# Kernel tuning notes

Hardware: AMD Instinct MI355X
Metric: run time of the kernel (lower is better)

Reference implementation:

```python
import jax, jax.numpy as jnp
import numpy as np

EPS = 1e-6


def _rms_norm(x, w):
    # RMSNorm over last dim in fp32, like Qwen3RMSNorm
    x32 = x.astype(jnp.float32)
    var = jnp.mean(x32 * x32, axis=-1, keepdims=True)
    return (x32 * jax.lax.rsqrt(var + EPS)).astype(x.dtype) * w


def _rotate_half(x):
    h = x.shape[-1] // 2
    return jnp.concatenate([-x[..., h:], x[..., :h]], axis=-1)


def setup_inputs() -> dict:
    key = jax.random.key(0)
    ks = jax.random.split(key, 8)
    B, S, HID = 1, 8192, 1024
    H, HKV, D = 16, 8, 128
    n_seg = 8
    hidden_states = jax.random.normal(ks[0], (B, S, HID), dtype=jnp.float32)
    cu_seqlens = jnp.arange(n_seg + 1, dtype=jnp.int32) * (S // n_seg)
    # multimodal RoPE tables: two position streams, each [B, S, D]
    inv_freq = 1.0 / (1e6 ** (jnp.arange(0, D, 2, dtype=jnp.float32) / D))
    pos = jnp.arange(S, dtype=jnp.float32)
    ang0 = pos[:, None] * inv_freq[None, :]            # [S, D/2]
    ang1 = (pos[:, None] * 0.5) * inv_freq[None, :]    # second stream
    def tab(a):
        return jnp.concatenate([a, a], axis=-1)[None]   # [1, S, D]
    cos = jnp.stack([tab(jnp.cos(ang0)), tab(jnp.cos(ang1))], axis=0)  # [2,1,S,D]
    sin = jnp.stack([tab(jnp.sin(ang0)), tab(jnp.sin(ang1))], axis=0)
    sd = 0.02
    Wq = jax.random.normal(ks[1], (H * D, HID), dtype=jnp.float32) * sd
    Wk = jax.random.normal(ks[2], (HKV * D, HID), dtype=jnp.float32) * sd
    Wv = jax.random.normal(ks[3], (HKV * D, HID), dtype=jnp.float32) * sd
    Wo = jax.random.normal(ks[4], (HID, H * D), dtype=jnp.float32) * sd
    q_norm_w = 1.0 + jax.random.normal(ks[5], (D,), dtype=jnp.float32) * sd
    k_norm_w = 1.0 + jax.random.normal(ks[6], (D,), dtype=jnp.float32) * sd
    return {"hidden_states": hidden_states, "cu_seqlens": cu_seqlens,
            "cos": cos, "sin": sin, "Wq": Wq, "Wk": Wk, "Wv": Wv, "Wo": Wo,
            "q_norm_w": q_norm_w, "k_norm_w": k_norm_w}


def reference(hidden_states, cu_seqlens, cos, sin, Wq, Wk, Wv, Wo, q_norm_w, k_norm_w):
    B, S, _ = hidden_states.shape
    D = q_norm_w.shape[0]
    H = Wq.shape[0] // D
    HKV = Wk.shape[0] // D
    groups = H // HKV
    n_seg = cu_seqlens.shape[0] - 1   # equal-length segments (static)
    L = S // n_seg
    scaling = D ** -0.5

    # projections -> [B, H(kv), S, D]
    q = (hidden_states @ Wq.T).reshape(B, S, H, D).transpose(0, 2, 1, 3)
    k = (hidden_states @ Wk.T).reshape(B, S, HKV, D).transpose(0, 2, 1, 3)
    v = (hidden_states @ Wv.T).reshape(B, S, HKV, D).transpose(0, 2, 1, 3)

    q = _rms_norm(q, q_norm_w)
    k = _rms_norm(k, k_norm_w)

    # multimodal RoPE: interleave the two streams across the two half-dims
    half = D // 2
    cos_e = jnp.concatenate([cos[0, ..., :half], cos[1, ..., half:]], axis=-1)[:, None]  # [B,1,S,D]
    sin_e = jnp.concatenate([sin[0, ..., :half], sin[1, ..., half:]], axis=-1)[:, None]
    q = q * cos_e + _rotate_half(q) * sin_e
    k = k * cos_e + _rotate_half(k) * sin_e

    # GQA: repeat kv heads
    k = jnp.repeat(k, groups, axis=1)
    v = jnp.repeat(v, groups, axis=1)

    # block-diagonal attention over cu_seqlens segments (equal-length -> reshape)
    qb = q.reshape(B, H, n_seg, L, D)
    kb = k.reshape(B, H, n_seg, L, D)
    vb = v.reshape(B, H, n_seg, L, D)
    scores = jnp.einsum('bhnld,bhnmd->bhnlm', qb, kb) * scaling
    probs = jax.nn.softmax(scores, axis=-1)
    ob = jnp.einsum('bhnlm,bhnmd->bhnld', probs, vb)
    out = ob.reshape(B, H, S, D).transpose(0, 2, 1, 3).reshape(B, S, H * D)
    return out @ Wo.T
```

## Files before the change

### kernel.cpp

```cpp
#include <hip/hip_runtime.h>

#define S_LEN 8192
#define HID   1024
#define NH    16
#define NKV   8
#define HD    128
#define LSEG  1024

typedef float  f4  __attribute__((ext_vector_type(4)));
typedef _Float16 h4 __attribute__((ext_vector_type(4)));
typedef _Float16 h8 __attribute__((ext_vector_type(8)));

__device__ __forceinline__ void gl_lds16(const void* g, void* l) {
  __builtin_amdgcn_global_load_lds((const __attribute__((address_space(1))) void*)g,
                                   (__attribute__((address_space(3))) void*)l, 16, 0, 0);
}

__device__ __forceinline__ h8 ld8u(const _Float16* p) {
  h4 a = *(const h4*)p;
  h4 b = *(const h4*)(p + 4);
  return __builtin_shufflevector(a, b, 0, 1, 2, 3, 4, 5, 6, 7);
}

template <int CTRL>
__device__ __forceinline__ float dppf(float v) {
  return __builtin_bit_cast(float,
      __builtin_amdgcn_mov_dpp(__builtin_bit_cast(int, v), CTRL, 0xF, 0xF, true));
}
__device__ __forceinline__ float red16_max(float x) {
  x = fmaxf(x, dppf<0xB1>(x));
  x = fmaxf(x, dppf<0x4E>(x));
  x = fmaxf(x, dppf<0x141>(x));
  x = fmaxf(x, dppf<0x140>(x));
  return x;
}
__device__ __forceinline__ float red16_sum(float x) {
  x += dppf<0xB1>(x);
  x += dppf<0x4E>(x);
  x += dppf<0x141>(x);
  x += dppf<0x140>(x);
  return x;
}

__global__ void convert_kernel(const float* __restrict__ hid, const float* __restrict__ wq,
                               const float* __restrict__ wk, const float* __restrict__ wv,
                               const float* __restrict__ wo,
                               _Float16* __restrict__ hid16, _Float16* __restrict__ wqkv,
                               _Float16* __restrict__ wo16) {
  const int total4 = 3670016;
  for (int i = blockIdx.x * blockDim.x + threadIdx.x; i < total4; i += gridDim.x * blockDim.x) {
    int i4 = i * 4;
    const float* src; _Float16* dst;
    if      (i4 <  8388608) { src = hid + i4;              dst = hid16 + i4; }
    else if (i4 < 10485760) { src = wq + (i4 -  8388608);  dst = wqkv + (i4 - 8388608); }
    else if (i4 < 11534336) { src = wk + (i4 - 10485760);  dst = wqkv + 2097152 + (i4 - 10485760); }
    else if (i4 < 12582912) { src = wv + (i4 - 11534336);  dst = wqkv + 3145728 + (i4 - 11534336); }
    else                    { src = wo + (i4 - 12582912);  dst = wo16 + (i4 - 12582912); }
    f4 x = *(const f4*)src;
    h4 y; y[0]=(_Float16)x[0]; y[1]=(_Float16)x[1]; y[2]=(_Float16)x[2]; y[3]=(_Float16)x[3];
    *(h4*)dst = y;
  }
}

template <int FUSED>
__global__ __launch_bounds__(256, 3)
void gemm_kernel(const _Float16* __restrict__ A, const _Float16* __restrict__ B,
                 float* __restrict__ Cout, int K, int N,
                 const float* __restrict__ cosp, const float* __restrict__ sinp,
                 const float* __restrict__ qnw, const float* __restrict__ knw,
                 _Float16* __restrict__ q16, _Float16* __restrict__ k16,
                 _Float16* __restrict__ v16T) {
  __shared__ __align__(16) char smem[32768];

  constexpr int GX  = FUSED ? 32 : 8;
  constexpr int NWG = FUSED ? 2048 : 512;
  const int lin = blockIdx.y * GX + blockIdx.x;
  const int swz = (lin & 7) * (NWG >> 3) + (lin >> 3);
  const int bx = swz & (GX - 1), by = swz / GX;

  const int tid = threadIdx.x, w = tid >> 6, ln = tid & 63;
  const int l15 = ln & 15, l4 = ln >> 4;
  const int m0 = by * 128, n0 = bx * 128;
  const int sg_row = ln >> 2, sg_cho = (ln & 3) * 8;

  f4 acc[2][8] = {};

  for (int k0 = 0; k0 < K; k0 += 64) {
    __syncthreads();
#pragma unroll
    for (int r = 0; r < 2; r++) {
      int ch = r * 4 + w;
#pragma unroll
      for (int u = 0; u < 2; u++) {
        gl_lds16(A + (size_t)(m0 + ch * 16 + sg_row) * K + k0 + u * 32 + sg_cho,
                 smem + u * 8192 + ch * 1024);
        gl_lds16(B + (size_t)(n0 + ch * 16 + sg_row) * K + k0 + u * 32 + sg_cho,
                 smem + 16384 + u * 8192 + ch * 1024);
      }
    }
    __syncthreads();
#pragma unroll
    for (int u = 0; u < 2; u++) {
      const _Float16* As = (const _Float16*)(smem + u * 8192);
      const _Float16* Bs = (const _Float16*)(smem + 16384 + u * 8192);
      h8 af[2], bf[8];
#pragma unroll
      for (int mt = 0; mt < 2; mt++) af[mt] = *(const h8*)(As + (w * 32 + mt * 16 + l15) * 32 + l4 * 8);
#pragma unroll
      for (int nt = 0; nt < 8; nt++) bf[nt] = *(const h8*)(Bs + (nt * 16 + l15) * 32 + l4 * 8);
#pragma unroll
      for (int mt = 0; mt < 2; mt++)
#pragma unroll
        for (int nt = 0; nt < 8; nt++)
          acc[mt][nt] = __builtin_amdgcn_mfma_f32_16x16x32_f16(af[mt], bf[nt], acc[mt][nt], 0, 0, 0);
    }
  }

  if (!FUSED) {
#pragma unroll
    for (int mt = 0; mt < 2; mt++)
#pragma unroll
      for (int rg = 0; rg < 4; rg++) {
        int row = m0 + w * 32 + mt * 16 + l4 * 4 + rg;
#pragma unroll
        for (int nt = 0; nt < 8; nt++)
          Cout[(size_t)row * N + n0 + nt * 16 + l15] = acc[mt][nt][rg];
      }
    return;
  } else {
    const int head = bx;
    if (head < 24) {
      const float* nw = (head < 16) ? qnw : knw;
      const float hs = (head < 16) ? 0.12751734f : 1.0f;
      _Float16* base = (head < 16) ? q16 + (size_t)head * S_LEN * HD
                                   : k16 + (size_t)(head - 16) * S_LEN * HD;
      float nwv[8];
#pragma unroll
      for (int nt = 0; nt < 8; nt++) nwv[nt] = nw[nt * 16 + l15];
#pragma unroll
      for (int mt = 0; mt < 2; mt++)
#pragma unroll
        for (int rg = 0; rg < 4; rg++) {
          const int row = m0 + w * 32 + mt * 16 + l4 * 4 + rg;
          float ss = 0.f;
#pragma unroll
          for (int nt = 0; nt < 8; nt++) ss += acc[mt][nt][rg] * acc[mt][nt][rg];
          ss = red16_sum(ss);
          const float sc = rsqrtf(ss * 0.0078125f + 1e-6f);
#pragma unroll
          for (int nt = 0; nt < 8; nt++) {
            const int c = nt * 16 + l15;
            const int str = (nt >= 4) ? 1048576 : 0;
            float x  = acc[mt][nt][rg] * sc * nwv[nt];
            float xp = acc[mt][nt ^ 4][rg] * sc * nwv[nt ^ 4];
            float ce = cosp[str + row * HD + c];
            float se = sinp[str + row * HD + c];
            float rot = (nt >= 4) ? xp : -xp;
            base[(size_t)row * HD + c] = (_Float16)((x * ce + rot * se) * hs);
          }
        }
    } else {
      _Float16* vb = v16T + (size_t)(head - 24) * S_LEN * HD;
#pragma unroll
      for (int mt = 0; mt < 2; mt++)
#pragma unroll
        for (int nt = 0; nt < 8; nt++) {
          h4 hv;
#pragma unroll
          for (int rg = 0; rg < 4; rg++) hv[rg] = (_Float16)acc[mt][nt][rg];
          *(h4*)&vb[(size_t)(nt * 16 + l15) * S_LEN + m0 + w * 32 + mt * 16 + l4 * 4] = hv;
        }
    }
  }
}

__global__ __launch_bounds__(256, 2)
void attn_kernel(const _Float16* __restrict__ q16, const _Float16* __restrict__ k16,
                 const _Float16* __restrict__ vT, _Float16* __restrict__ ao16) {
  const int bid = blockIdx.x;
  const int xcd = bid & 7, slot = bid >> 3;
  const int grp = xcd * 8 + (slot >> 4);
  const int mem = slot & 15;
  const int g = grp >> 3, hkv = grp & 7;
  const int tq = mem & 7, h = hkv * 2 + (mem >> 3);

  const int tid = threadIdx.x, w = tid >> 6, ln = tid & 63;
  const int l15 = ln & 15, l4 = ln >> 4;

  __shared__ _Float16 Qs[128 * 132];
  __shared__ _Float16 KP[128 * 68];
  __shared__ _Float16 Vt[128 * 68];

  const _Float16* qsrc = q16 + ((size_t)h * S_LEN + g * LSEG + tq * 128) * HD;
#pragma unroll
  for (int i = 0; i < 8; i++) {
    int c = tid + 256 * i, row = c >> 4, o = c & 15;
    uint4 v = *(const uint4*)(qsrc + row * HD + o * 8);
    *(uint2*)&Qs[row * 132 + o * 8]     = make_uint2(v.x, v.y);
    *(uint2*)&Qs[row * 132 + o * 8 + 4] = make_uint2(v.z, v.w);
  }

  f4 O[2][8] = {};
  float mr[2][4], lr[2][4];
#pragma unroll
  for (int mt = 0; mt < 2; mt++)
#pragma unroll
    for (int rg = 0; rg < 4; rg++) { mr[mt][rg] = -1e30f; lr[mt][rg] = 0.f; }

  const size_t kbase = ((size_t)hkv * S_LEN + g * LSEG) * HD;
  const size_t vbase = (size_t)hkv * S_LEN * HD + (size_t)g * LSEG;

  const int krow = tid >> 4, ko = tid & 15;
  const int vd   = tid >> 3, vo = tid & 7;

  uint4 kr[4], vr[4];
#pragma unroll
  for (int i = 0; i < 4; i++) {
    kr[i] = *(const uint4*)(k16 + kbase + (size_t)(krow + 16 * i) * HD + ko * 8);
    vr[i] = *(const uint4*)(vT + vbase + (size_t)(vd + 32 * i) * S_LEN + vo * 8);
  }
#pragma unroll
  for (int i = 0; i < 4; i++) {
    int row = krow + 16 * i;
    *(uint2*)&KP[row * 132 + ko * 8]     = make_uint2(kr[i].x, kr[i].y);
    *(uint2*)&KP[row * 132 + ko * 8 + 4] = make_uint2(kr[i].z, kr[i].w);
    int d = vd + 32 * i;
    *(uint2*)&Vt[d * 68 + vo * 8]     = make_uint2(vr[i].x, vr[i].y);
    *(uint2*)&Vt[d * 68 + vo * 8 + 4] = make_uint2(vr[i].z, vr[i].w);
  }

  for (int j = 0; j < 16; j++) {
    __syncthreads();

    const int jn = (j + 1) & 15;
#pragma unroll
    for (int i = 0; i < 4; i++) {
      kr[i] = *(const uint4*)(k16 + kbase + (size_t)(jn * 64 + krow + 16 * i) * HD + ko * 8);
      vr[i] = *(const uint4*)(vT + vbase + (size_t)(vd + 32 * i) * S_LEN + jn * 64 + vo * 8);
    }

    f4 s[2][4] = {};
#pragma unroll
    for (int kk = 0; kk < 4; kk++) {
      h8 a0 = ld8u(Qs + (w * 32 + l15) * 132 + kk * 32 + l4 * 8);
      h8 a1 = ld8u(Qs + (w * 32 + 16 + l15) * 132 + kk * 32 + l4 * 8);
#pragma unroll
      for (int nt = 0; nt < 4; nt++) {
        h8 b = ld8u(KP + (nt * 16 + l15) * 132 + kk * 32 + l4 * 8);
        s[0][nt] = __builtin_amdgcn_mfma_f32_16x16x32_f16(a0, b, s[0][nt], 0, 0, 0);
        s[1][nt] = __builtin_amdgcn_mfma_f32_16x16x32_f16(a1, b, s[1][nt], 0, 0, 0);
      }
    }

    float mx[2][4];
    bool nd = false;
#pragma unroll
    for (int mt = 0; mt < 2; mt++)
#pragma unroll
      for (int rg = 0; rg < 4; rg++) {
        float m = fmaxf(fmaxf(s[mt][0][rg], s[mt][1][rg]), fmaxf(s[mt][2][rg], s[mt][3][rg]));
        m = red16_max(m);
        mx[mt][rg] = m;
        nd = nd || (m > mr[mt][rg] + 8.f);
      }
    const bool needr = __any((int)nd) != 0;
    float al[2][4];
    if (needr) {
#pragma unroll
      for (int mt = 0; mt < 2; mt++)
#pragma unroll
        for (int rg = 0; rg < 4; rg++) {
          float mnew = fmaxf(mr[mt][rg], mx[mt][rg]);
          al[mt][rg] = exp2f(mr[mt][rg] - mnew);
          mr[mt][rg] = mnew;
        }
    }
#pragma unroll
    for (int mt = 0; mt < 2; mt++)
#pragma unroll
      for (int rg = 0; rg < 4; rg++) {
        float rs = 0.f;
#pragma unroll
        for (int nt = 0; nt < 4; nt++) {
          float p = exp2f(s[mt][nt][rg] - mr[mt][rg]);
          s[mt][nt][rg] = p;
          rs += p;
        }
        rs = red16_sum(rs);
        if (needr) lr[mt][rg] = lr[mt][rg] * al[mt][rg] + rs;
        else       lr[mt][rg] += rs;
      }

    __syncthreads();
#pragma unroll
    for (int mt = 0; mt < 2; mt++)
#pragma unroll
      for (int nt = 0; nt < 4; nt++)
#pragma unroll
        for (int rg = 0; rg < 4; rg++)
          KP[(w * 32 + mt * 16 + l4 * 4 + rg) * 68 + nt * 16 + l15] = (_Float16)s[mt][nt][rg];
    if (needr) {
#pragma unroll
      for (int mt = 0; mt < 2; mt++)
#pragma unroll
        for (int d8 = 0; d8 < 8; d8++)
#pragma unroll
          for (int rg = 0; rg < 4; rg++) O[mt][d8][rg] *= al[mt][rg];
    }
    __syncthreads();

#pragma unroll
    for (int kk = 0; kk < 2; kk++) {
      h8 a0 = ld8u(KP + (w * 32 + l15) * 68 + kk * 32 + l4 * 8);
      h8 a1 = ld8u(KP + (w * 32 + 16 + l15) * 68 + kk * 32 + l4 * 8);
#pragma unroll
      for (int d8 = 0; d8 < 8; d8++) {
        h8 b = ld8u(Vt + (d8 * 16 + l15) * 68 + kk * 32 + l4 * 8);
        O[0][d8] = __builtin_amdgcn_mfma_f32_16x16x32_f16(a0, b, O[0][d8], 0, 0, 0);
        O[1][d8] = __builtin_amdgcn_mfma_f32_16x16x32_f16(a1, b, O[1][d8], 0, 0, 0);
      }
    }

    __syncthreads();
#pragma unroll
    for (int i = 0; i < 4; i++) {
      int row = krow + 16 * i;
      *(uint2*)&KP[row * 132 + ko * 8]     = make_uint2(kr[i].x, kr[i].y);
      *(uint2*)&KP[row * 132 + ko * 8 + 4] = make_uint2(kr[i].z, kr[i].w);
      int d = vd + 32 * i;
      *(uint2*)&Vt[d * 68 + vo * 8]     = make_uint2(vr[i].x, vr[i].y);
      *(uint2*)&Vt[d * 68 + vo * 8 + 4] = make_uint2(vr[i].z, vr[i].w);
    }
  }

  const size_t obase = (size_t)(g * LSEG + tq * 128);
#pragma unroll
  for (int mt = 0; mt < 2; mt++)
#pragma unroll
    for (int rg = 0; rg < 4; rg++) {
      float inv = 1.f / lr[mt][rg];
#pragma unroll
      for (int d8 = 0; d8 < 8; d8++)
        ao16[(obase + w * 32 + mt * 16 + l4 * 4 + rg) * 2048 + h * HD + d8 * 16 + l15] =
            (_Float16)(O[mt][d8][rg] * inv);
    }
}

extern "C" void kernel_launch(void* const* d_in, const int* in_sizes, int n_in,
                              void* d_out, int out_size, void* d_ws, size_t ws_size,
                              hipStream_t stream) {
  const float* hid  = (const float*)d_in[0];
  const float* cosp = (const float*)d_in[2];
  const float* sinp = (const float*)d_in[3];
  const float* wq   = (const float*)d_in[4];
  const float* wk   = (const float*)d_in[5];
  const float* wv   = (const float*)d_in[6];
  const float* wo   = (const float*)d_in[7];
  const float* qnw  = (const float*)d_in[8];
  const float* knw  = (const float*)d_in[9];
  float* out = (float*)d_out;

  _Float16* hid16 = (_Float16*)d_ws;
  _Float16* wqkv  = hid16 + 8388608;
  _Float16* wo16  = wqkv + 4194304;
  _Float16* q16   = wo16 + 2097152;
  _Float16* k16   = q16 + 16777216;
  _Float16* v16T  = k16 + 8388608;
  _Float16* ao16  = v16T + 8388608;

  convert_kernel<<<dim3(1024), dim3(256), 0, stream>>>(hid, wq, wk, wv, wo, hid16, wqkv, wo16);
  gemm_kernel<1><<<dim3(32, 64), dim3(256), 0, stream>>>(hid16, wqkv, nullptr, 1024, 4096,
                                                         cosp, sinp, qnw, knw, q16, k16, v16T);
  attn_kernel<<<dim3(1024), dim3(256), 0, stream>>>(q16, k16, v16T, ao16);
  gemm_kernel<0><<<dim3(8, 64), dim3(256), 0, stream>>>(ao16, wo16, out, 2048, 1024,
                                                        nullptr, nullptr, nullptr, nullptr,
                                                        nullptr, nullptr, nullptr);
}
```

Measured before the change: 405.4 us.

## Read K and tiled V directly from global memory in attention, dropping LDS staging

The V projection epilogue now writes V transposed in 64-key tiles of [128 x 64], so each attention step reads a contiguous block. The attention kernel drops the register-prefetch plus LDS staging of K and V, loads MFMA B-operands straight from global/L2, and removes most block barriers. Only the per-warp P tile stays in LDS, which lowers LDS use and allows the launch bound to rise to three blocks per CU. The trade-off is that every wave re-fetches K/V from cache with no explicit prefetch, which adds global-load latency inside the MFMA loop.

```diff
diff --git a/kernel.cpp b/kernel.cpp
--- a/kernel.cpp
+++ b/kernel.cpp
@@ -168,13 +168,15 @@
           h4 hv;
 #pragma unroll
           for (int rg = 0; rg < 4; rg++) hv[rg] = (_Float16)acc[mt][nt][rg];
-          *(h4*)&vb[(size_t)(nt * 16 + l15) * S_LEN + m0 + w * 32 + mt * 16 + l4 * 4] = hv;
+          const int s = m0 + w * 32 + mt * 16 + l4 * 4;
+          const int t = s >> 6, l = s & 63, d = nt * 16 + l15;
+          *(h4*)&vb[((size_t)t * 128 + d) * 64 + l] = hv;
         }
     }
   }
 }
 
-__global__ __launch_bounds__(256, 2)
+__global__ __launch_bounds__(256, 3)
 void attn_kernel(const _Float16* __restrict__ q16, const _Float16* __restrict__ k16,
                  const _Float16* __restrict__ vT, _Float16* __restrict__ ao16) {
   const int bid = blockIdx.x;
@@ -188,8 +190,7 @@
   const int l15 = ln & 15, l4 = ln >> 4;
 
   __shared__ _Float16 Qs[128 * 132];
-  __shared__ _Float16 KP[128 * 68];
-  __shared__ _Float16 Vt[128 * 68];
+  __shared__ _Float16 Ps[128 * 68];
 
   const _Float16* qsrc = q16 + ((size_t)h * S_LEN + g * LSEG + tq * 128) * HD;
 #pragma unroll
@@ -207,38 +208,13 @@
 #pragma unroll
     for (int rg = 0; rg < 4; rg++) { mr[mt][rg] = -1e30f; lr[mt][rg] = 0.f; }
 
-  const size_t kbase = ((size_t)hkv * S_LEN + g * LSEG) * HD;
-  const size_t vbase = (size_t)hkv * S_LEN * HD + (size_t)g * LSEG;
-
-  const int krow = tid >> 4, ko = tid & 15;
-  const int vd   = tid >> 3, vo = tid & 7;
-
-  uint4 kr[4], vr[4];
-#pragma unroll
-  for (int i = 0; i < 4; i++) {
-    kr[i] = *(const uint4*)(k16 + kbase + (size_t)(krow + 16 * i) * HD + ko * 8);
-    vr[i] = *(const uint4*)(vT + vbase + (size_t)(vd + 32 * i) * S_LEN + vo * 8);
-  }
-#pragma unroll
-  for (int i = 0; i < 4; i++) {
-    int row = krow + 16 * i;
-    *(uint2*)&KP[row * 132 + ko * 8]     = make_uint2(kr[i].x, kr[i].y);
-    *(uint2*)&KP[row * 132 + ko * 8 + 4] = make_uint2(kr[i].z, kr[i].w);
-    int d = vd + 32 * i;
-    *(uint2*)&Vt[d * 68 + vo * 8]     = make_uint2(vr[i].x, vr[i].y);
-    *(uint2*)&Vt[d * 68 + vo * 8 + 4] = make_uint2(vr[i].z, vr[i].w);
-  }
+  const _Float16* kseg = k16 + ((size_t)hkv * S_LEN + g * LSEG) * HD;
+  const _Float16* vseg = vT + (size_t)hkv * S_LEN * HD + (size_t)g * 16 * 8192;
+
+  __syncthreads();
 
   for (int j = 0; j < 16; j++) {
-    __syncthreads();
-
-    const int jn = (j + 1) & 15;
-#pragma unroll
-    for (int i = 0; i < 4; i++) {
-      kr[i] = *(const uint4*)(k16 + kbase + (size_t)(jn * 64 + krow + 16 * i) * HD + ko * 8);
-      vr[i] = *(const uint4*)(vT + vbase + (size_t)(vd + 32 * i) * S_LEN + jn * 64 + vo * 8);
-    }
-
+    const _Float16* kt = kseg + (size_t)j * 64 * HD;
     f4 s[2][4] = {};
 #pragma unroll
     for (int kk = 0; kk < 4; kk++) {
@@ -246,7 +222,7 @@
       h8 a1 = ld8u(Qs + (w * 32 + 16 + l15) * 132 + kk * 32 + l4 * 8);
 #pragma unroll
       for (int nt = 0; nt < 4; nt++) {
-        h8 b = ld8u(KP + (nt * 16 + l15) * 132 + kk * 32 + l4 * 8);
+        h8 b = *(const h8*)(kt + (nt * 16 + l15) * HD + kk * 32 + l4 * 8);
         s[0][nt] = __builtin_amdgcn_mfma_f32_16x16x32_f16(a0, b, s[0][nt], 0, 0, 0);
         s[1][nt] = __builtin_amdgcn_mfma_f32_16x16x32_f16(a1, b, s[1][nt], 0, 0, 0);
       }
@@ -291,14 +267,13 @@
         else       lr[mt][rg] += rs;
       }
 
-    __syncthreads();
 #pragma unroll
     for (int mt = 0; mt < 2; mt++)
 #pragma unroll
       for (int nt = 0; nt < 4; nt++)
 #pragma unroll
         for (int rg = 0; rg < 4; rg++)
-          KP[(w * 32 + mt * 16 + l4 * 4 + rg) * 68 + nt * 16 + l15] = (_Float16)s[mt][nt][rg];
+          Ps[(w * 32 + mt * 16 + l4 * 4 + rg) * 68 + nt * 16 + l15] = (_Float16)s[mt][nt][rg];
     if (needr) {
 #pragma unroll
       for (int mt = 0; mt < 2; mt++)
@@ -307,29 +282,18 @@
 #pragma unroll
           for (int rg = 0; rg < 4; rg++) O[mt][d8][rg] *= al[mt][rg];
     }
-    __syncthreads();
-
+
+    const _Float16* vt = vseg + (size_t)(g * 0 + j) * 8192;
 #pragma unroll
     for (int kk = 0; kk < 2; kk++) {
-      h8 a0 = ld8u(KP + (w * 32 + l15) * 68 + kk * 32 + l4 * 8);
-      h8 a1 = ld8u(KP + (w * 32 + 16 + l15) * 68 + kk * 32 + l4 * 8);
+      h8 a0 = ld8u(Ps + (w * 32 + l15) * 68 + kk * 32 + l4 * 8);
+      h8 a1 = ld8u(Ps + (w * 32 + 16 + l15) * 68 + kk * 32 + l4 * 8);
 #pragma unroll
       for (int d8 = 0; d8 < 8; d8++) {
-        h8 b = ld8u(Vt + (d8 * 16 + l15) * 68 + kk * 32 + l4 * 8);
+        h8 b = *(const h8*)(vt + (d8 * 16 + l15) * 64 + kk * 32 + l4 * 8);
         O[0][d8] = __builtin_amdgcn_mfma_f32_16x16x32_f16(a0, b, O[0][d8], 0, 0, 0);
         O[1][d8] = __builtin_amdgcn_mfma_f32_16x16x32_f16(a1, b, O[1][d8], 0, 0, 0);
       }
-    }
-
-    __syncthreads();
-#pragma unroll
-    for (int i = 0; i < 4; i++) {
-      int row = krow + 16 * i;
-      *(uint2*)&KP[row * 132 + ko * 8]     = make_uint2(kr[i].x, kr[i].y);
-      *(uint2*)&KP[row * 132 + ko * 8 + 4] = make_uint2(kr[i].z, kr[i].w);
-      int d = vd + 32 * i;
-      *(uint2*)&Vt[d * 68 + vo * 8]     = make_uint2(vr[i].x, vr[i].y);
-      *(uint2*)&Vt[d * 68 + vo * 8 + 4] = make_uint2(vr[i].z, vr[i].w);
     }
   }
 
```

New measurement: 588.4 us. 45.1% more time.
